# Kernel tuning notes

Measured on AMD Instinct MI355X. Metric: run time of the kernel, lower is better.

## Reference

```python
import jax, jax.numpy as jnp
import numpy as np
import math

B, C1, H, W, D, NH = 32, 128, 32, 32, 256, 8
KS = 9
GLOBAL_RATIO = 0.0005
K_CH = 8


def setup_inputs() -> dict:
    key = jax.random.key(0)
    ks = jax.random.split(key, 6)
    s = 1.0 / math.sqrt(D)
    return {
        "x": jax.random.normal(ks[0], (B, 1, H, W), jnp.float32),
        "conv_w": jax.random.normal(ks[1], (C1, 1, KS, KS), jnp.float32) * 0.05,
        "channel_embed": jax.random.normal(ks[2], (C1, D), jnp.float32),
        "in_proj_w": jax.random.normal(ks[3], (3 * D, D), jnp.float32) * s,
        "in_proj_b": jnp.zeros((3 * D,), jnp.float32),
        "out_proj_w": jax.random.normal(ks[4], (D, D), jnp.float32) * s,
        "out_proj_b": jnp.zeros((D,), jnp.float32),
    }


def _pos_encoding(h, w, d):
    # Faithful to the torch code: the (H, d/2) sin/cos source broadcasts against
    # the trailing (W, d/2) dims of the (H,W,d/2) slice, so the PE varies only
    # along the W axis (requires H == W, which holds here).
    div = jnp.exp(jnp.arange(0, d, 2, dtype=jnp.float32) * (-math.log(10000.0) / d))
    ang = jnp.arange(w, dtype=jnp.float32)[:, None] * div          # (W, d/2)
    pe_w = jnp.stack([jnp.sin(ang), jnp.cos(ang)], axis=-1).reshape(w, d)
    return jnp.broadcast_to(pe_w[None], (h, w, d))                 # (H, W, d)


def _forward(x, conv_w, channel_embed, in_proj_w, in_proj_b, out_proj_w, out_proj_b):
    A = jax.nn.relu(jax.lax.conv_general_dilated(
        x, conv_w, window_strides=(1, 1),
        padding=[(KS // 2, KS // 2), (KS // 2, KS // 2)],
        dimension_numbers=("NCHW", "OIHW", "NCHW")))                # (B,C,H,W)
    Bb, C, Hh, Ww = A.shape
    k = max(1, int(math.ceil(GLOBAL_RATIO * C * Hh * Ww)))          # = 66

    # global top-k threshold mask over flattened activations
    A_flat = A.reshape(Bb, -1)
    topk_vals, _ = jax.lax.top_k(A_flat, k)
    thresh = topk_vals[:, -1][:, None]
    mask_global = (A_flat >= thresh).reshape(A.shape)
    A_global = A * mask_global.astype(A.dtype)

    # per-pixel channel top-8 + scatter
    v = jnp.transpose(A_global, (0, 2, 3, 1))                       # (B,H,W,C)
    topv, topi = jax.lax.top_k(v, K_CH)                             # (B,H,W,8)
    logits = (jax.nn.one_hot(topi, C, dtype=v.dtype) * topv[..., None]).sum(axis=-2)

    # global max normalization per batch element
    gmax = jnp.max(logits.reshape(Bb, -1), axis=1)[:, None, None, None]
    denom = jnp.where(gmax == 0, jnp.float32(1.0), gmax)
    sparse_weights = jnp.where(gmax == 0, jnp.float32(0.0), logits / denom)

    # channel-embedding projection + 2D positional encoding
    loc_emb = jnp.einsum('bhwc,cd->bhwd', sparse_weights, channel_embed)
    loc_emb = loc_emb + _pos_encoding(Hh, Ww, D)[None]
    seq = loc_emb.reshape(Bb, Hh * Ww, D)                           # (B, S, D)

    # nn.MultiheadAttention (batch_first) self-attention
    qkv = seq @ in_proj_w.T + in_proj_b
    q, kk, vv = jnp.split(qkv, 3, axis=-1)
    dh = D // NH
    heads = lambda t: t.reshape(Bb, -1, NH, dh).transpose(0, 2, 1, 3)
    q, kk, vv = heads(q), heads(kk), heads(vv)
    scores = jnp.einsum('bhqd,bhkd->bhqk', q, kk) / math.sqrt(dh)
    attn = jax.nn.softmax(scores, axis=-1)
    ctx = jnp.einsum('bhqk,bhkd->bhqd', attn, vv)
    ctx = ctx.transpose(0, 2, 1, 3).reshape(Bb, -1, D)
    attn_out = ctx @ out_proj_w.T + out_proj_b                      # (B, S, D)

    pooled = attn_out.mean(axis=1)                                  # (B, D)
    return pooled, sparse_weights, topi


def reference(x, conv_w, channel_embed, in_proj_w, in_proj_b, out_proj_w, out_proj_b):
    return _forward(x, conv_w, channel_embed, in_proj_w, in_proj_b,
                    out_proj_w, out_proj_b)
```

## Files before the change

### kernel.cpp

```cpp
#include <hip/hip_runtime.h>
#include <hip/hip_bf16.h>

#define BB 32
#define C1 128
#define SS 1024
#define DD 256
#define NHH 8
#define DHH 32
#define KSEL 66
#define TRIPLE 768
#define NTOK 80
#define SCAPS 128
#define CCAP 2048
#define DMAX (32 + NTOK)
#define PEROW (BB * NTOK)
#define SELFLAG 0x40000000u

typedef __attribute__((ext_vector_type(8))) short bf16x8;
typedef __attribute__((ext_vector_type(4))) float f32x4;

__device__ inline short f2bf(float f) {
  union { __hip_bfloat16 h; unsigned short u; } c;
  c.h = __float2bfloat16(f);
  return (short)c.u;
}
__device__ inline float pe_val(int w, int d) {
  int i2 = d >> 1;
  float dv = expf((float)(2 * i2) * (-9.210340371976184f / 256.f));
  float ang = (float)w * dv;
  return (d & 1) ? cosf(ang) : sinf(ang);
}

__global__ __launch_bounds__(256) void zero_kernel(
    unsigned* __restrict__ ghist1, unsigned* __restrict__ selv,
    unsigned* __restrict__ gmaxb) {
  const int b = blockIdx.x, t = threadIdx.x;
  uint4* g = (uint4*)(ghist1 + b * 2048);
  uint4 z = {0u, 0u, 0u, 0u};
  g[t] = z;
  g[t + 256] = z;
  if (t == 0) { selv[b] = 0u; gmaxb[b] = 0u; }
}

__global__ __launch_bounds__(256) void conv_relu_hist_kernel(
    const float* __restrict__ x, const float* __restrict__ w, float* __restrict__ A,
    unsigned* __restrict__ ghist1, unsigned* __restrict__ gmaxb,
    float* __restrict__ out_topi, float* __restrict__ out_sw) {
  const int bx = blockIdx.x;
  const int b = bx >> 6, c0 = (bx & 63) * 2;
  __shared__ float xs[40 * 40];
  __shared__ unsigned h[2048];
  __shared__ unsigned smax;
  const int t = threadIdx.x;
  {
    float4 z = {0.f, 0.f, 0.f, 0.f};
    float4* sw4 = (float4*)(out_sw + (size_t)bx * 2048);
    sw4[t] = z;
    sw4[t + 256] = z;
  }
  if (bx < 256) {
    int k0 = bx * 1024 + t * 4;
    float4 v = (k0 & 4) ? make_float4(4.f, 5.f, 6.f, 7.f)
                        : make_float4(0.f, 1.f, 2.f, 3.f);
    *(float4*)&out_topi[k0] = v;
  }
  for (int i = t; i < 1600; i += 256) {
    int r = i / 40, cc = i - r * 40;
    int gi = r - 4, gj = cc - 4;
    float v = 0.f;
    if (gi >= 0 && gi < 32 && gj >= 0 && gj < 32) v = x[(size_t)b * 1024 + gi * 32 + gj];
    xs[i] = v;
  }
  for (int i = t; i < 2048; i += 256) h[i] = 0u;
  if (t == 0) smax = 0u;
  __syncthreads();
  const float* w0 = w + (size_t)c0 * 81;
  const float* w1 = w0 + 81;
  const int r = t >> 3, cbase = (t & 7) * 4;
  const float4* xs4 = (const float4*)xs;
  float a0 = 0.f, a1 = 0.f, a2 = 0.f, a3 = 0.f;
  float b0 = 0.f, b1 = 0.f, b2 = 0.f, b3 = 0.f;
#pragma unroll
  for (int u = 0; u < 9; ++u) {
    int base4 = (r + u) * 10 + (t & 7);
    float4 xA = xs4[base4];
    float4 xB = xs4[base4 + 1];
    float4 xC = xs4[base4 + 2];
    float xv[12] = {xA.x, xA.y, xA.z, xA.w, xB.x, xB.y, xB.z, xB.w,
                    xC.x, xC.y, xC.z, xC.w};
#pragma unroll
    for (int v = 0; v < 9; ++v) {
      float f0 = w0[u * 9 + v], f1 = w1[u * 9 + v];
      a0 += f0 * xv[v];     a1 += f0 * xv[v + 1];
      a2 += f0 * xv[v + 2]; a3 += f0 * xv[v + 3];
      b0 += f1 * xv[v];     b1 += f1 * xv[v + 1];
      b2 += f1 * xv[v + 2]; b3 += f1 * xv[v + 3];
    }
  }
  a0 = fmaxf(a0, 0.f); a1 = fmaxf(a1, 0.f); a2 = fmaxf(a2, 0.f); a3 = fmaxf(a3, 0.f);
  b0 = fmaxf(b0, 0.f); b1 = fmaxf(b1, 0.f); b2 = fmaxf(b2, 0.f); b3 = fmaxf(b3, 0.f);
  float4 va = {a0, a1, a2, a3}, vb = {b0, b1, b2, b3};
  *(float4*)&A[((size_t)(b * C1 + c0) << 10) + r * 32 + cbase] = va;
  *(float4*)&A[((size_t)(b * C1 + c0 + 1) << 10) + r * 32 + cbase] = vb;
  unsigned lmax = 0u;
#pragma unroll
  for (int k = 0; k < 8; ++k) {
    float f = (k == 0) ? a0 : (k == 1) ? a1 : (k == 2) ? a2 : (k == 3) ? a3
            : (k == 4) ? b0 : (k == 5) ? b1 : (k == 6) ? b2 : b3;
    unsigned bits = __float_as_uint(f);
    if (bits > lmax) lmax = bits;
    if (bits >= (1u << 21)) atomicAdd(&h[bits >> 21], 1u);
  }
  atomicMax(&smax, lmax);
  __syncthreads();
  for (int i = t; i < 2048; i += 256)
    if (h[i]) atomicAdd(&ghist1[b * 2048 + i], h[i]);
  if (t == 0) atomicMax(&gmaxb[b], smax);
}

__global__ __launch_bounds__(1024) void sel_kernel(
    const unsigned* __restrict__ gh, unsigned* __restrict__ selv,
    unsigned* __restrict__ cnd_n, float* __restrict__ ctx) {
  const int b = blockIdx.x, t = threadIdx.x;
  __shared__ unsigned hl[2048];
  __shared__ unsigned sfx[1024];
  if (t < 256) ctx[b * DD + t] = 0.f;
  if (t == 0) cnd_n[b * 32] = 0u;
  unsigned r = (unsigned)KSEL;
  hl[t] = gh[b * 2048 + t];
  hl[t + 1024] = gh[b * 2048 + t + 1024];
  __syncthreads();
  sfx[t] = hl[2 * t] + hl[2 * t + 1];
  __syncthreads();
  for (int off = 1; off < 1024; off <<= 1) {
    unsigned v = (t + off < 1024) ? sfx[t + off] : 0u;
    __syncthreads();
    sfx[t] += v;
    __syncthreads();
  }
  if (sfx[0] < r) {
    if (t == 0) selv[b] = SELFLAG;
    return;
  }
  unsigned Snext = (t < 1023) ? sfx[t + 1] : 0u;
  unsigned hi = hl[2 * t + 1], lo = hl[2 * t];
  if (Snext < r && Snext + hi >= r) selv[b] = (unsigned)(2 * t + 1);
  else if (Snext + hi < r && Snext + hi + lo >= r) selv[b] = (unsigned)(2 * t);
}

__global__ __launch_bounds__(256) void gather_kernel(
    const float* __restrict__ A, const unsigned* __restrict__ selv,
    unsigned* __restrict__ cnd_n, float* __restrict__ candv,
    unsigned* __restrict__ candloc) {
  const int b = blockIdx.y, slice = blockIdx.x, t = threadIdx.x;
  const unsigned v1 = selv[b];
  if (v1 == SELFLAG) return;
  const unsigned thr = v1 << 21;
  __shared__ float lv[512];
  __shared__ unsigned ll[512];
  __shared__ unsigned lcnt, gbase;
  if (t == 0) lcnt = 0u;
  __syncthreads();
  const float4* Ab = (const float4*)(A + (size_t)b * (C1 * SS) + slice * 2048);
  const float4 va = Ab[t];
  const float4 vb = Ab[t + 256];
  const int base = slice * 2048 + t * 4;
  const float f[8] = {va.x, va.y, va.z, va.w, vb.x, vb.y, vb.z, vb.w};
#pragma unroll
  for (int c = 0; c < 8; ++c) {
    if (__float_as_uint(f[c]) >= thr) {
      unsigned loc = (unsigned)(base + (c < 4 ? c : 1020 + c));
      unsigned s = atomicAdd(&lcnt, 1u);
      if (s < 512u) {
        lv[s] = f[c];
        ll[s] = loc;
      } else {
        unsigned g = atomicAdd(&cnd_n[b * 32], 1u);
        if (g < (unsigned)CCAP) {
          candv[b * CCAP + g] = f[c];
          candloc[b * CCAP + g] = loc;
        }
      }
    }
  }
  __syncthreads();
  const unsigned cnt = lcnt < 512u ? lcnt : 512u;
  if (t == 0 && cnt) gbase = atomicAdd(&cnd_n[b * 32], cnt);
  __syncthreads();
  for (unsigned u = t; u < cnt; u += 256) {
    unsigned s = gbase + u;
    if (s < (unsigned)CCAP) {
      candv[b * CCAP + s] = lv[u];
      candloc[b * CCAP + s] = ll[u];
    }
  }
}

__global__ __launch_bounds__(256) void sparse_pixels_kernel(
    const unsigned* __restrict__ cnd_n, const float* __restrict__ candv,
    const unsigned* __restrict__ candloc, const unsigned* __restrict__ selv,
    const float* __restrict__ gmaxp, float* __restrict__ out_sw,
    float* __restrict__ out_topi, int* __restrict__ kidx8,
    float* __restrict__ kval8, unsigned* __restrict__ glist,
    unsigned* __restrict__ nswb, unsigned* __restrict__ npix) {
  const int b = blockIdx.x, t = threadIdx.x;
  __shared__ float cv[CCAP];
  __shared__ unsigned cl[CCAP];
  __shared__ float sv[SCAPS];
  __shared__ int sch[SCAPS], spx[SCAPS];
  __shared__ int s_n_sh;
  __shared__ unsigned pixbit[32];
  __shared__ int mcount[NTOK];
  __shared__ int leadp[NTOK];
  if (t == 0) s_n_sh = 0;
  if (t < 32) pixbit[t] = 0u;
  unsigned n = cnd_n[b * 32];
  if (n > (unsigned)CCAP) n = (unsigned)CCAP;
  const bool ok = (selv[b] != SELFLAG) && (n >= (unsigned)KSEL);
  for (unsigned i = t; i < n; i += 256) {
    cv[i] = candv[b * CCAP + i];
    cl[i] = candloc[b * CCAP + i];
  }
  __syncthreads();
  if (ok) {
    for (unsigned i = t; i < n; i += 256) {
      float v = cv[i];
      int g = 0;
      for (unsigned j = 0; j < n; ++j) g += (cv[j] > v);
      if (g < KSEL) {
        int k = atomicAdd(&s_n_sh, 1);
        if (k < SCAPS) {
          sv[k] = v;
          sch[k] = (int)(cl[i] >> 10);
          spx[k] = (int)(cl[i] & 1023u);
        }
      }
    }
  }
  __syncthreads();
  const int s_n = s_n_sh < SCAPS ? s_n_sh : SCAPS;
  for (int i = t; i < s_n; i += 256)
    atomicOr(&pixbit[spx[i] >> 5], 1u << (spx[i] & 31));
  __syncthreads();
  if (t == 0) {
    int np = 0;
#pragma unroll
    for (int wd = 0; wd < 32; ++wd) np += __popc(pixbit[wd]);
    npix[b] = (unsigned)(np < NTOK ? np : NTOK);
  }
  if (t < 32) {
    unsigned cnt = 0;
#pragma unroll
    for (int rr = 0; rr < 32; ++rr) cnt += (pixbit[rr] >> t) & 1u;
    nswb[b * 32 + t] = cnt;
  }
  const float gm = gmaxp[b];
  const float scale = gm > 0.f ? 1.f / gm : 0.f;
  __syncthreads();
  for (int i = t; i < s_n; i += 256) {
    const int p = spx[i];
    const float v = sv[i];
    const int c = sch[i];
    const int word = p >> 5, bit = p & 31;
    int slot = 0;
    for (int wd = 0; wd < word; ++wd) slot += __popc(pixbit[wd]);
    slot += __popc(pixbit[word] & (bit ? ((1u << bit) - 1u) : 0u));
    if (slot >= NTOK) continue;
    int rank = 0, cntp = 0;
    for (int j = 0; j < s_n; ++j) {
      if (spx[j] != p) continue;
      ++cntp;
      rank += (sv[j] > v || (sv[j] == v && sch[j] < c));
    }
    const size_t pix = (size_t)b * SS + p;
    const float sval = v * scale;
    if (rank < 8) {
      out_topi[pix * 8 + rank] = (float)c;
      out_sw[pix * C1 + c] = sval;
      kidx8[((size_t)b * NTOK + slot) * 8 + rank] = c;
      kval8[((size_t)b * NTOK + slot) * 8 + rank] = sval;
    }
    if (rank == 0) {
      glist[b * NTOK + slot] =
          ((unsigned)b << 16) | ((unsigned)slot << 8) | (unsigned)(p & 31);
      mcount[slot] = cntp < 8 ? cntp : 8;
      leadp[slot] = p;
    }
  }
  __syncthreads();
  const int np = (int)npix[b];
  for (int s = t; s < np; s += 256) {
    const int m = mcount[s];
    if (m >= 8) continue;
    const int p = leadp[s];
    int used[8];
    for (int k = 0; k < m; ++k) used[k] = kidx8[((size_t)b * NTOK + s) * 8 + k];
    int fill_c = 0;
    for (int j = m; j < 8; ++j) {
      bool adv = true;
      while (adv) {
        adv = false;
        for (int k = 0; k < m; ++k)
          if (used[k] == fill_c) adv = true;
        if (adv) ++fill_c;
      }
      kidx8[((size_t)b * NTOK + s) * 8 + j] = fill_c;
      kval8[((size_t)b * NTOK + s) * 8 + j] = 0.f;
      out_topi[((size_t)b * SS + p) * 8 + j] = (float)fill_c;
      ++fill_c;
    }
  }
}

__global__ __launch_bounds__(256) void emb_build_kernel(
    const unsigned* __restrict__ npix, const int* __restrict__ kidx8,
    const float* __restrict__ kval8, const unsigned* __restrict__ glist,
    const float* __restrict__ emb, float* __restrict__ E) {
  const int bx = blockIdx.x;
  const int d = threadIdx.x;
  if (bx >= PEROW) {
    E[(size_t)bx * DD + d] = pe_val(bx - PEROW, d);
    return;
  }
  const int b = bx / NTOK, i = bx - b * NTOK;
  if ((unsigned)i >= npix[b]) return;
  const int w = (int)(glist[bx] & 255u);
  const int* ki = kidx8 + (size_t)bx * 8;
  const float* kv = kval8 + (size_t)bx * 8;
  float e = pe_val(w, d);
#pragma unroll
  for (int j = 0; j < 8; ++j) e += kv[j] * emb[(size_t)ki[j] * DD + d];
  E[(size_t)bx * DD + d] = e;
}

__global__ __launch_bounds__(256) void eqkv_gemm_kernel(
    const float* __restrict__ E, const float* __restrict__ W,
    const float* __restrict__ bias, float* __restrict__ SQKV) {
  __shared__ __align__(16) short As[128][40];
  __shared__ __align__(16) short Bs[128][40];
  const int mt = blockIdx.x / 6, nt = blockIdx.x % 6;
  const int t = threadIdx.x;
  const int wv = t >> 6, lane = t & 63, lg = lane >> 4, ln = lane & 15;
  const int wm = wv >> 1, wn = wv & 1;

  f32x4 acc[4][4];
#pragma unroll
  for (int i = 0; i < 4; ++i)
#pragma unroll
    for (int j = 0; j < 4; ++j) acc[i][j] = (f32x4){0, 0, 0, 0};

  for (int k0 = 0; k0 < DD; k0 += 32) {
    __syncthreads();
    for (int f = t; f < 1024; f += 256) {
      int row = f >> 3, q4 = (f & 7) * 4;
      float4 xa = *(const float4*)&E[(size_t)(mt * 128 + row) * DD + k0 + q4];
      float4 wa = *(const float4*)&W[(size_t)(nt * 128 + row) * DD + k0 + q4];
      short* ad = &As[row][q4];
      ad[0] = f2bf(xa.x); ad[1] = f2bf(xa.y); ad[2] = f2bf(xa.z); ad[3] = f2bf(xa.w);
      short* bd = &Bs[row][q4];
      bd[0] = f2bf(wa.x); bd[1] = f2bf(wa.y); bd[2] = f2bf(wa.z); bd[3] = f2bf(wa.w);
    }
    __syncthreads();
    bf16x8 af[4], bfr[4];
#pragma unroll
    for (int i = 0; i < 4; ++i) af[i] = *(const bf16x8*)&As[wm * 64 + i * 16 + ln][lg * 8];
#pragma unroll
    for (int j = 0; j < 4; ++j) bfr[j] = *(const bf16x8*)&Bs[wn * 64 + j * 16 + ln][lg * 8];
#pragma unroll
    for (int i = 0; i < 4; ++i)
#pragma unroll
      for (int j = 0; j < 4; ++j)
        acc[i][j] = __builtin_amdgcn_mfma_f32_16x16x32_bf16(af[i], bfr[j], acc[i][j], 0, 0, 0);
  }
#pragma unroll
  for (int i = 0; i < 4; ++i) {
#pragma unroll
    for (int j = 0; j < 4; ++j) {
      int col = nt * 128 + wn * 64 + j * 16 + ln;
      float bcol = bias[col];
#pragma unroll
      for (int r = 0; r < 4; ++r) {
        int row = mt * 128 + wm * 64 + i * 16 + lg * 4 + r;
        SQKV[(size_t)row * TRIPLE + col] = acc[i][j][r] + bcol;
      }
    }
  }
}

__global__ __launch_bounds__(256) void attn_small_kernel(
    const float* __restrict__ SQKV, const unsigned* __restrict__ npix,
    const unsigned* __restrict__ nswb, float* __restrict__ ctx_sum) {
  const int blk = blockIdx.x;
  const int qg = blk & 3, h = (blk >> 2) & 7, b = blk >> 5;
  const int nsb = (int)npix[b];
  const int D = 32 + nsb;
  if (qg * 32 >= D) return;
  const int t = threadIdx.x;
  __shared__ float Kh[DMAX][36];
  __shared__ float Vh[DMAX][36];
  __shared__ float cw[DMAX];
  __shared__ float sctx[32];
  const int hoff = h * DHH;
  for (int idx = t; idx < D * 32; idx += 256) {
    int j = idx >> 5, d = idx & 31;
    int row = (j < 32) ? (PEROW + j) : (b * NTOK + j - 32);
    const float* src = &SQKV[(size_t)row * TRIPLE];
    Kh[j][d] = src[DD + hoff + d];
    Vh[j][d] = src[2 * DD + hoff + d];
  }
  if (t < D) cw[t] = (t < 32) ? (float)(32 - (int)nswb[b * 32 + t]) : 1.0f;
  if (t < 32) sctx[t] = 0.f;
  __syncthreads();

  const int q = qg * 32 + (t >> 3);
  const int g = t & 7;
  const bool act = (q < D);
  float m = -1e30f, l = 0.f;
  float acc[32];
#pragma unroll
  for (int d = 0; d < 32; ++d) acc[d] = 0.f;
  if (act) {
    const float qsc = 0.25506973f;
    int qrow = (q < 32) ? (PEROW + q) : (b * NTOK + q - 32);
    const float* qsrc = &SQKV[(size_t)qrow * TRIPLE];
    float qv[32];
#pragma unroll
    for (int d = 0; d < 32; ++d) qv[d] = qsrc[hoff + d] * qsc;
#pragma unroll 1
    for (int j = g; j < D; j += 8) {
      float s = 0.f;
      const float* kr = &Kh[j][0];
#pragma unroll
      for (int d = 0; d < 32; ++d) s += qv[d] * kr[d];
      float mn = fmaxf(m, s);
      float corr = exp2f(m - mn);
      float pw = cw[j] * exp2f(s - mn);
      l = l * corr + pw;
      const float* vr = &Vh[j][0];
#pragma unroll
      for (int d = 0; d < 32; ++d) acc[d] = acc[d] * corr + pw * vr[d];
      m = mn;
    }
  }
#pragma unroll
  for (int off = 1; off <= 4; off <<= 1) {
    float mo = __shfl_xor(m, off);
    float lo = __shfl_xor(l, off);
    float mm = fmaxf(m, mo);
    float fa = exp2f(m - mm), fb = exp2f(mo - mm);
    l = l * fa + lo * fb;
#pragma unroll
    for (int d = 0; d < 32; ++d) {
      float ao = __shfl_xor(acc[d], off);
      acc[d] = acc[d] * fa + ao * fb;
    }
    m = mm;
  }
  const float wq = (act && l > 0.f) ? cw[q] / l : 0.f;
#pragma unroll
  for (int d = 0; d < 32; ++d) {
    float val = wq * acc[d];
    val += __shfl_xor(val, 8);
    val += __shfl_xor(val, 16);
    val += __shfl_xor(val, 32);
    if ((t & 63) == 0) atomicAdd(&sctx[d], val);
  }
  __syncthreads();
  if (t < 32) atomicAdd(&ctx_sum[b * DD + hoff + t], sctx[t]);
}

__global__ __launch_bounds__(256) void pooled_kernel(
    const float* __restrict__ ctx_sum, const float* __restrict__ Wout,
    const float* __restrict__ bout, float* __restrict__ out) {
  const int b = blockIdx.x;
  const int o = threadIdx.x;
  __shared__ float mc[DD];
  mc[o] = ctx_sum[b * DD + o] * (1.f / 1024.f);
  __syncthreads();
  float acc = bout[o];
  const float* wr = Wout + (size_t)o * DD;
#pragma unroll 4
  for (int d = 0; d < DD; ++d) acc += mc[d] * wr[d];
  out[b * DD + o] = acc;
}

extern "C" void kernel_launch(void* const* d_in, const int* in_sizes, int n_in,
                              void* d_out, int out_size, void* d_ws, size_t ws_size,
                              hipStream_t stream) {
  const float* x = (const float*)d_in[0];
  const float* conv_w = (const float*)d_in[1];
  const float* emb = (const float*)d_in[2];
  const float* ipw = (const float*)d_in[3];
  const float* ipb = (const float*)d_in[4];
  const float* opw = (const float*)d_in[5];
  const float* opb = (const float*)d_in[6];

  float* out = (float*)d_out;
  float* out_pooled = out;
  float* out_sw = out + 8192;
  float* out_topi = out + 8192 + 4194304;

  char* ws = (char*)d_ws;
  float*    A      = (float*)(ws);
  unsigned* ghist1 = (unsigned*)(ws + 16777216);
  unsigned* selv   = (unsigned*)(ws + 17039360);
  unsigned* gmaxb  = (unsigned*)(ws + 17039488);
  unsigned* nswb   = (unsigned*)(ws + 17039616);
  unsigned* npix   = (unsigned*)(ws + 17043712);
  unsigned* glist  = (unsigned*)(ws + 17043840);
  unsigned* cnd_n  = (unsigned*)(ws + 17054080);
  float*    candv  = (float*)(ws + 17058176);
  unsigned* candloc= (unsigned*)(ws + 17320320);
  int*      kidx8  = (int*)(ws + 17582464);
  float*    kval8  = (float*)(ws + 17664384);
  float*    E      = (float*)(ws + 17746304);
  float*    SQKV   = (float*)(ws + 20498816);
  float*    ctx    = (float*)(ws + 28756352);

  zero_kernel<<<BB, 256, 0, stream>>>(ghist1, selv, gmaxb);
  conv_relu_hist_kernel<<<BB * 64, 256, 0, stream>>>(x, conv_w, A, ghist1, gmaxb,
                                                     out_topi, out_sw);
  sel_kernel<<<BB, 1024, 0, stream>>>(ghist1, selv, cnd_n, ctx);
  gather_kernel<<<dim3(64, BB), 256, 0, stream>>>(A, selv, cnd_n, candv, candloc);
  sparse_pixels_kernel<<<BB, 256, 0, stream>>>(cnd_n, candv, candloc, selv,
                                               (const float*)gmaxb, out_sw, out_topi,
                                               kidx8, kval8, glist, nswb, npix);
  emb_build_kernel<<<PEROW + 32, 256, 0, stream>>>(npix, kidx8, kval8, glist, emb, E);
  eqkv_gemm_kernel<<<21 * 6, 256, 0, stream>>>(E, ipw, ipb, SQKV);
  attn_small_kernel<<<BB * NHH * 4, 256, 0, stream>>>(SQKV, npix, nswb, ctx);
  pooled_kernel<<<BB, 256, 0, stream>>>(ctx, opw, opb, out_pooled);
}
```

Measured before the change: 129.9 us.

## Fuse selection, sparse-pixel and pooling stages via last-block-done counters

```diff
diff --git a/kernel.cpp b/kernel.cpp
--- a/kernel.cpp
+++ b/kernel.cpp
@@ -30,27 +30,48 @@
   float ang = (float)w * dv;
   return (d & 1) ? cosf(ang) : sinf(ang);
 }
+__device__ inline unsigned aload_u(const unsigned* p) {
+  return __hip_atomic_load(p, __ATOMIC_RELAXED, __HIP_MEMORY_SCOPE_AGENT);
+}
+__device__ inline float aload_f(const float* p) {
+  return __hip_atomic_load(p, __ATOMIC_RELAXED, __HIP_MEMORY_SCOPE_AGENT);
+}
+__device__ inline void astore_u(unsigned* p, unsigned v) {
+  __hip_atomic_store(p, v, __ATOMIC_RELAXED, __HIP_MEMORY_SCOPE_AGENT);
+}
+__device__ inline void astore_f(float* p, float v) {
+  __hip_atomic_store(p, v, __ATOMIC_RELAXED, __HIP_MEMORY_SCOPE_AGENT);
+}
 
 __global__ __launch_bounds__(256) void zero_kernel(
     unsigned* __restrict__ ghist1, unsigned* __restrict__ selv,
-    unsigned* __restrict__ gmaxb) {
+    unsigned* __restrict__ gmaxb, unsigned* __restrict__ cnd_n,
+    unsigned* __restrict__ ccnt, unsigned* __restrict__ gcnt,
+    unsigned* __restrict__ acnt, float* __restrict__ ctx) {
   const int b = blockIdx.x, t = threadIdx.x;
   uint4* g = (uint4*)(ghist1 + b * 2048);
   uint4 z = {0u, 0u, 0u, 0u};
   g[t] = z;
   g[t + 256] = z;
-  if (t == 0) { selv[b] = 0u; gmaxb[b] = 0u; }
+  ctx[b * DD + t] = 0.f;
+  if (t == 0) {
+    selv[b] = 0u; gmaxb[b] = 0u; cnd_n[b * 32] = 0u;
+    ccnt[b * 32] = 0u; gcnt[b * 32] = 0u; acnt[b * 32] = 0u;
+  }
 }
 
 __global__ __launch_bounds__(256) void conv_relu_hist_kernel(
     const float* __restrict__ x, const float* __restrict__ w, float* __restrict__ A,
     unsigned* __restrict__ ghist1, unsigned* __restrict__ gmaxb,
-    float* __restrict__ out_topi, float* __restrict__ out_sw) {
+    float* __restrict__ out_topi, float* __restrict__ out_sw,
+    unsigned* __restrict__ ccnt, unsigned* __restrict__ selv) {
   const int bx = blockIdx.x;
   const int b = bx >> 6, c0 = (bx & 63) * 2;
   __shared__ float xs[40 * 40];
   __shared__ unsigned h[2048];
+  __shared__ unsigned gsum[256];
   __shared__ unsigned smax;
+  __shared__ unsigned lastf;
   const int t = threadIdx.x;
   {
     float4 z = {0.f, 0.f, 0.f, 0.f};
@@ -116,94 +137,49 @@
   for (int i = t; i < 2048; i += 256)
     if (h[i]) atomicAdd(&ghist1[b * 2048 + i], h[i]);
   if (t == 0) atomicMax(&gmaxb[b], smax);
-}
-
-__global__ __launch_bounds__(1024) void sel_kernel(
-    const unsigned* __restrict__ gh, unsigned* __restrict__ selv,
-    unsigned* __restrict__ cnd_n, float* __restrict__ ctx) {
-  const int b = blockIdx.x, t = threadIdx.x;
-  __shared__ unsigned hl[2048];
-  __shared__ unsigned sfx[1024];
-  if (t < 256) ctx[b * DD + t] = 0.f;
-  if (t == 0) cnd_n[b * 32] = 0u;
-  unsigned r = (unsigned)KSEL;
-  hl[t] = gh[b * 2048 + t];
-  hl[t + 1024] = gh[b * 2048 + t + 1024];
-  __syncthreads();
-  sfx[t] = hl[2 * t] + hl[2 * t + 1];
-  __syncthreads();
-  for (int off = 1; off < 1024; off <<= 1) {
-    unsigned v = (t + off < 1024) ? sfx[t + off] : 0u;
-    __syncthreads();
-    sfx[t] += v;
-    __syncthreads();
-  }
-  if (sfx[0] < r) {
+  __threadfence();
+  if (t == 0) lastf = atomicAdd(&ccnt[b * 32], 1u);
+  __syncthreads();
+  if (lastf != 63u) return;
+  for (int i = t; i < 2048; i += 256)
+    h[i] = aload_u(&ghist1[b * 2048 + i]);
+  __syncthreads();
+  unsigned hv[8], T = 0;
+#pragma unroll
+  for (int k = 0; k < 8; ++k) { hv[k] = h[t * 8 + k]; T += hv[k]; }
+  gsum[t] = T;
+  __syncthreads();
+  for (int off = 1; off < 256; off <<= 1) {
+    unsigned v = (t + off < 256) ? gsum[t + off] : 0u;
+    __syncthreads();
+    gsum[t] += v;
+    __syncthreads();
+  }
+  if (gsum[0] < (unsigned)KSEL) {
     if (t == 0) selv[b] = SELFLAG;
     return;
   }
-  unsigned Snext = (t < 1023) ? sfx[t + 1] : 0u;
-  unsigned hi = hl[2 * t + 1], lo = hl[2 * t];
-  if (Snext < r && Snext + hi >= r) selv[b] = (unsigned)(2 * t + 1);
-  else if (Snext + hi < r && Snext + hi + lo >= r) selv[b] = (unsigned)(2 * t);
+  unsigned run = (t < 255) ? gsum[t + 1] : 0u;
+#pragma unroll
+  for (int k = 7; k >= 0; --k) {
+    unsigned Sb = run + hv[k];
+    if (run < (unsigned)KSEL && Sb >= (unsigned)KSEL) selv[b] = (unsigned)(t * 8 + k);
+    run = Sb;
+  }
 }
 
 __global__ __launch_bounds__(256) void gather_kernel(
     const float* __restrict__ A, const unsigned* __restrict__ selv,
     unsigned* __restrict__ cnd_n, float* __restrict__ candv,
-    unsigned* __restrict__ candloc) {
-  const int b = blockIdx.y, slice = blockIdx.x, t = threadIdx.x;
-  const unsigned v1 = selv[b];
-  if (v1 == SELFLAG) return;
-  const unsigned thr = v1 << 21;
-  __shared__ float lv[512];
-  __shared__ unsigned ll[512];
-  __shared__ unsigned lcnt, gbase;
-  if (t == 0) lcnt = 0u;
-  __syncthreads();
-  const float4* Ab = (const float4*)(A + (size_t)b * (C1 * SS) + slice * 2048);
-  const float4 va = Ab[t];
-  const float4 vb = Ab[t + 256];
-  const int base = slice * 2048 + t * 4;
-  const float f[8] = {va.x, va.y, va.z, va.w, vb.x, vb.y, vb.z, vb.w};
-#pragma unroll
-  for (int c = 0; c < 8; ++c) {
-    if (__float_as_uint(f[c]) >= thr) {
-      unsigned loc = (unsigned)(base + (c < 4 ? c : 1020 + c));
-      unsigned s = atomicAdd(&lcnt, 1u);
-      if (s < 512u) {
-        lv[s] = f[c];
-        ll[s] = loc;
-      } else {
-        unsigned g = atomicAdd(&cnd_n[b * 32], 1u);
-        if (g < (unsigned)CCAP) {
-          candv[b * CCAP + g] = f[c];
-          candloc[b * CCAP + g] = loc;
-        }
-      }
-    }
-  }
-  __syncthreads();
-  const unsigned cnt = lcnt < 512u ? lcnt : 512u;
-  if (t == 0 && cnt) gbase = atomicAdd(&cnd_n[b * 32], cnt);
-  __syncthreads();
-  for (unsigned u = t; u < cnt; u += 256) {
-    unsigned s = gbase + u;
-    if (s < (unsigned)CCAP) {
-      candv[b * CCAP + s] = lv[u];
-      candloc[b * CCAP + s] = ll[u];
-    }
-  }
-}
-
-__global__ __launch_bounds__(256) void sparse_pixels_kernel(
-    const unsigned* __restrict__ cnd_n, const float* __restrict__ candv,
-    const unsigned* __restrict__ candloc, const unsigned* __restrict__ selv,
-    const float* __restrict__ gmaxp, float* __restrict__ out_sw,
+    unsigned* __restrict__ candloc, unsigned* __restrict__ gcnt,
+    const unsigned* __restrict__ gmaxb, float* __restrict__ out_sw,
     float* __restrict__ out_topi, int* __restrict__ kidx8,
     float* __restrict__ kval8, unsigned* __restrict__ glist,
     unsigned* __restrict__ nswb, unsigned* __restrict__ npix) {
-  const int b = blockIdx.x, t = threadIdx.x;
+  const int b = blockIdx.y, slice = blockIdx.x, t = threadIdx.x;
+  __shared__ float lv[512];
+  __shared__ unsigned ll[512];
+  __shared__ unsigned lcnt, gbase, glast;
   __shared__ float cv[CCAP];
   __shared__ unsigned cl[CCAP];
   __shared__ float sv[SCAPS];
@@ -212,14 +188,57 @@
   __shared__ unsigned pixbit[32];
   __shared__ int mcount[NTOK];
   __shared__ int leadp[NTOK];
+  const unsigned v1 = selv[b];
+  if (v1 != SELFLAG) {
+    if (t == 0) lcnt = 0u;
+    __syncthreads();
+    const unsigned thr = v1 << 21;
+    const float4* Ab = (const float4*)(A + (size_t)b * (C1 * SS) + slice * 2048);
+    const float4 va = Ab[t];
+    const float4 vb = Ab[t + 256];
+    const int base = slice * 2048 + t * 4;
+    const float f[8] = {va.x, va.y, va.z, va.w, vb.x, vb.y, vb.z, vb.w};
+#pragma unroll
+    for (int c = 0; c < 8; ++c) {
+      if (__float_as_uint(f[c]) >= thr) {
+        unsigned loc = (unsigned)(base + (c < 4 ? c : 1020 + c));
+        unsigned s = atomicAdd(&lcnt, 1u);
+        if (s < 512u) {
+          lv[s] = f[c];
+          ll[s] = loc;
+        } else {
+          unsigned g = atomicAdd(&cnd_n[b * 32], 1u);
+          if (g < (unsigned)CCAP) {
+            astore_f(&candv[b * CCAP + g], f[c]);
+            astore_u(&candloc[b * CCAP + g], loc);
+          }
+        }
+      }
+    }
+    __syncthreads();
+    const unsigned cnt = lcnt < 512u ? lcnt : 512u;
+    if (t == 0 && cnt) gbase = atomicAdd(&cnd_n[b * 32], cnt);
+    __syncthreads();
+    for (unsigned u = t; u < cnt; u += 256) {
+      unsigned s = gbase + u;
+      if (s < (unsigned)CCAP) {
+        astore_f(&candv[b * CCAP + s], lv[u]);
+        astore_u(&candloc[b * CCAP + s], ll[u]);
+      }
+    }
+  }
+  __threadfence();
+  if (t == 0) glast = atomicAdd(&gcnt[b * 32], 1u);
+  __syncthreads();
+  if (glast != 63u) return;
   if (t == 0) s_n_sh = 0;
   if (t < 32) pixbit[t] = 0u;
-  unsigned n = cnd_n[b * 32];
+  unsigned n = aload_u(&cnd_n[b * 32]);
   if (n > (unsigned)CCAP) n = (unsigned)CCAP;
-  const bool ok = (selv[b] != SELFLAG) && (n >= (unsigned)KSEL);
+  const bool ok = (v1 != SELFLAG) && (n >= (unsigned)KSEL);
   for (unsigned i = t; i < n; i += 256) {
-    cv[i] = candv[b * CCAP + i];
-    cl[i] = candloc[b * CCAP + i];
+    cv[i] = aload_f(&candv[b * CCAP + i]);
+    cl[i] = aload_u(&candloc[b * CCAP + i]);
   }
   __syncthreads();
   if (ok) {
@@ -249,12 +268,12 @@
     npix[b] = (unsigned)(np < NTOK ? np : NTOK);
   }
   if (t < 32) {
-    unsigned cnt = 0;
-#pragma unroll
-    for (int rr = 0; rr < 32; ++rr) cnt += (pixbit[rr] >> t) & 1u;
-    nswb[b * 32 + t] = cnt;
-  }
-  const float gm = gmaxp[b];
+    unsigned cnt2 = 0;
+#pragma unroll
+    for (int rr = 0; rr < 32; ++rr) cnt2 += (pixbit[rr] >> t) & 1u;
+    nswb[b * 32 + t] = cnt2;
+  }
+  const float gm = __uint_as_float(gmaxb[b]);
   const float scale = gm > 0.f ? 1.f / gm : 0.f;
   __syncthreads();
   for (int i = t; i < s_n; i += 256) {
@@ -389,99 +408,99 @@
 
 __global__ __launch_bounds__(256) void attn_small_kernel(
     const float* __restrict__ SQKV, const unsigned* __restrict__ npix,
-    const unsigned* __restrict__ nswb, float* __restrict__ ctx_sum) {
+    const unsigned* __restrict__ nswb, float* __restrict__ ctx_sum,
+    unsigned* __restrict__ acnt, const float* __restrict__ opw,
+    const float* __restrict__ opb, float* __restrict__ out_pooled) {
   const int blk = blockIdx.x;
   const int qg = blk & 3, h = (blk >> 2) & 7, b = blk >> 5;
   const int nsb = (int)npix[b];
   const int D = 32 + nsb;
-  if (qg * 32 >= D) return;
   const int t = threadIdx.x;
   __shared__ float Kh[DMAX][36];
   __shared__ float Vh[DMAX][36];
   __shared__ float cw[DMAX];
   __shared__ float sctx[32];
-  const int hoff = h * DHH;
-  for (int idx = t; idx < D * 32; idx += 256) {
-    int j = idx >> 5, d = idx & 31;
-    int row = (j < 32) ? (PEROW + j) : (b * NTOK + j - 32);
-    const float* src = &SQKV[(size_t)row * TRIPLE];
-    Kh[j][d] = src[DD + hoff + d];
-    Vh[j][d] = src[2 * DD + hoff + d];
-  }
-  if (t < D) cw[t] = (t < 32) ? (float)(32 - (int)nswb[b * 32 + t]) : 1.0f;
-  if (t < 32) sctx[t] = 0.f;
-  __syncthreads();
-
-  const int q = qg * 32 + (t >> 3);
-  const int g = t & 7;
-  const bool act = (q < D);
-  float m = -1e30f, l = 0.f;
-  float acc[32];
-#pragma unroll
-  for (int d = 0; d < 32; ++d) acc[d] = 0.f;
-  if (act) {
-    const float qsc = 0.25506973f;
-    int qrow = (q < 32) ? (PEROW + q) : (b * NTOK + q - 32);
-    const float* qsrc = &SQKV[(size_t)qrow * TRIPLE];
-    float qv[32];
-#pragma unroll
-    for (int d = 0; d < 32; ++d) qv[d] = qsrc[hoff + d] * qsc;
+  __shared__ unsigned alast;
+  __shared__ float mcp[DD];
+  if (qg * 32 < D) {
+    const int hoff = h * DHH;
+    for (int idx = t; idx < D * 32; idx += 256) {
+      int j = idx >> 5, d = idx & 31;
+      int row = (j < 32) ? (PEROW + j) : (b * NTOK + j - 32);
+      const float* src = &SQKV[(size_t)row * TRIPLE];
+      Kh[j][d] = src[DD + hoff + d];
+      Vh[j][d] = src[2 * DD + hoff + d];
+    }
+    if (t < D) cw[t] = (t < 32) ? (float)(32 - (int)nswb[b * 32 + t]) : 1.0f;
+    if (t < 32) sctx[t] = 0.f;
+    __syncthreads();
+    const int q = qg * 32 + (t >> 3);
+    const int g = t & 7;
+    const bool act = (q < D);
+    float m = -1e30f, l = 0.f;
+    float acc[32];
+#pragma unroll
+    for (int d = 0; d < 32; ++d) acc[d] = 0.f;
+    if (act) {
+      const float qsc = 0.25506973f;
+      int qrow = (q < 32) ? (PEROW + q) : (b * NTOK + q - 32);
+      const float* qsrc = &SQKV[(size_t)qrow * TRIPLE];
+      float qv[32];
+#pragma unroll
+      for (int d = 0; d < 32; ++d) qv[d] = qsrc[hoff + d] * qsc;
 #pragma unroll 1
-    for (int j = g; j < D; j += 8) {
-      float s = 0.f;
-      const float* kr = &Kh[j][0];
-#pragma unroll
-      for (int d = 0; d < 32; ++d) s += qv[d] * kr[d];
-      float mn = fmaxf(m, s);
-      float corr = exp2f(m - mn);
-      float pw = cw[j] * exp2f(s - mn);
-      l = l * corr + pw;
-      const float* vr = &Vh[j][0];
-#pragma unroll
-      for (int d = 0; d < 32; ++d) acc[d] = acc[d] * corr + pw * vr[d];
-      m = mn;
-    }
-  }
-#pragma unroll
-  for (int off = 1; off <= 4; off <<= 1) {
-    float mo = __shfl_xor(m, off);
-    float lo = __shfl_xor(l, off);
-    float mm = fmaxf(m, mo);
-    float fa = exp2f(m - mm), fb = exp2f(mo - mm);
-    l = l * fa + lo * fb;
+      for (int j = g; j < D; j += 8) {
+        float s = 0.f;
+        const float* kr = &Kh[j][0];
+#pragma unroll
+        for (int d = 0; d < 32; ++d) s += qv[d] * kr[d];
+        float mn = fmaxf(m, s);
+        float corr = exp2f(m - mn);
+        float pw = cw[j] * exp2f(s - mn);
+        l = l * corr + pw;
+        const float* vr = &Vh[j][0];
+#pragma unroll
+        for (int d = 0; d < 32; ++d) acc[d] = acc[d] * corr + pw * vr[d];
+        m = mn;
+      }
+    }
+#pragma unroll
+    for (int off = 1; off <= 4; off <<= 1) {
+      float mo = __shfl_xor(m, off);
+      float lo = __shfl_xor(l, off);
+      float mm = fmaxf(m, mo);
+      float fa = exp2f(m - mm), fb = exp2f(mo - mm);
+      l = l * fa + lo * fb;
+#pragma unroll
+      for (int d = 0; d < 32; ++d) {
+        float ao = __shfl_xor(acc[d], off);
+        acc[d] = acc[d] * fa + ao * fb;
+      }
+      m = mm;
+    }
+    const float wq = (act && l > 0.f) ? cw[q] / l : 0.f;
 #pragma unroll
     for (int d = 0; d < 32; ++d) {
-      float ao = __shfl_xor(acc[d], off);
-      acc[d] = acc[d] * fa + ao * fb;
-    }
-    m = mm;
-  }
-  const float wq = (act && l > 0.f) ? cw[q] / l : 0.f;
-#pragma unroll
-  for (int d = 0; d < 32; ++d) {
-    float val = wq * acc[d];
-    val += __shfl_xor(val, 8);
-    val += __shfl_xor(val, 16);
-    val += __shfl_xor(val, 32);
-    if ((t & 63) == 0) atomicAdd(&sctx[d], val);
-  }
-  __syncthreads();
-  if (t < 32) atomicAdd(&ctx_sum[b * DD + hoff + t], sctx[t]);
-}
-
-__global__ __launch_bounds__(256) void pooled_kernel(
-    const float* __restrict__ ctx_sum, const float* __restrict__ Wout,
-    const float* __restrict__ bout, float* __restrict__ out) {
-  const int b = blockIdx.x;
-  const int o = threadIdx.x;
-  __shared__ float mc[DD];
-  mc[o] = ctx_sum[b * DD + o] * (1.f / 1024.f);
-  __syncthreads();
-  float acc = bout[o];
-  const float* wr = Wout + (size_t)o * DD;
+      float val = wq * acc[d];
+      val += __shfl_xor(val, 8);
+      val += __shfl_xor(val, 16);
+      val += __shfl_xor(val, 32);
+      if ((t & 63) == 0) atomicAdd(&sctx[d], val);
+    }
+    __syncthreads();
+    if (t < 32) atomicAdd(&ctx_sum[b * DD + hoff + t], sctx[t]);
+  }
+  __threadfence();
+  if (t == 0) alast = atomicAdd(&acnt[b * 32], 1u);
+  __syncthreads();
+  if (alast != 31u) return;
+  mcp[t] = aload_f(&ctx_sum[b * DD + t]) * (1.f / 1024.f);
+  __syncthreads();
+  float pacc = opb[t];
+  const float* wr = opw + (size_t)t * DD;
 #pragma unroll 4
-  for (int d = 0; d < DD; ++d) acc += mc[d] * wr[d];
-  out[b * DD + o] = acc;
+  for (int d = 0; d < DD; ++d) pacc += mcp[d] * wr[d];
+  out_pooled[b * DD + t] = pacc;
 }
 
 extern "C" void kernel_launch(void* const* d_in, const int* in_sizes, int n_in,
@@ -509,24 +528,25 @@
   unsigned* npix   = (unsigned*)(ws + 17043712);
   unsigned* glist  = (unsigned*)(ws + 17043840);
   unsigned* cnd_n  = (unsigned*)(ws + 17054080);
-  float*    candv  = (float*)(ws + 17058176);
-  unsigned* candloc= (unsigned*)(ws + 17320320);
-  int*      kidx8  = (int*)(ws + 17582464);
-  float*    kval8  = (float*)(ws + 17664384);
-  float*    E      = (float*)(ws + 17746304);
-  float*    SQKV   = (float*)(ws + 20498816);
-  float*    ctx    = (float*)(ws + 28756352);
-
-  zero_kernel<<<BB, 256, 0, stream>>>(ghist1, selv, gmaxb);
+  unsigned* ccnt   = (unsigned*)(ws + 17058176);
+  unsigned* gcnt   = (unsigned*)(ws + 17062272);
+  unsigned* acnt   = (unsigned*)(ws + 17066368);
+  float*    candv  = (float*)(ws + 17070464);
+  unsigned* candloc= (unsigned*)(ws + 17332608);
+  int*      kidx8  = (int*)(ws + 17594752);
+  float*    kval8  = (float*)(ws + 17676672);
+  float*    E      = (float*)(ws + 17758592);
+  float*    SQKV   = (float*)(ws + 20511104);
+  float*    ctx    = (float*)(ws + 28768640);
+
+  zero_kernel<<<BB, 256, 0, stream>>>(ghist1, selv, gmaxb, cnd_n, ccnt, gcnt, acnt, ctx);
   conv_relu_hist_kernel<<<BB * 64, 256, 0, stream>>>(x, conv_w, A, ghist1, gmaxb,
-                                                     out_topi, out_sw);
-  sel_kernel<<<BB, 1024, 0, stream>>>(ghist1, selv, cnd_n, ctx);
-  gather_kernel<<<dim3(64, BB), 256, 0, stream>>>(A, selv, cnd_n, candv, candloc);
-  sparse_pixels_kernel<<<BB, 256, 0, stream>>>(cnd_n, candv, candloc, selv,
-                                               (const float*)gmaxb, out_sw, out_topi,
-                                               kidx8, kval8, glist, nswb, npix);
+                                                     out_topi, out_sw, ccnt, selv);
+  gather_kernel<<<dim3(64, BB), 256, 0, stream>>>(A, selv, cnd_n, candv, candloc,
+                                                  gcnt, gmaxb, out_sw, out_topi,
+                                                  kidx8, kval8, glist, nswb, npix);
   emb_build_kernel<<<PEROW + 32, 256, 0, stream>>>(npix, kidx8, kval8, glist, emb, E);
   eqkv_gemm_kernel<<<21 * 6, 256, 0, stream>>>(E, ipw, ipb, SQKV);
-  attn_small_kernel<<<BB * NHH * 4, 256, 0, stream>>>(SQKV, npix, nswb, ctx);
-  pooled_kernel<<<BB, 256, 0, stream>>>(ctx, opw, opb, out_pooled);
-}
+  attn_small_kernel<<<BB * NHH * 4, 256, 0, stream>>>(SQKV, npix, nswb, ctx,
+                                                      acnt, opw, opb, out_pooled);
+}
```

Result: slower. 483.8 us (+272.3%).
